# Optimization experiments

Hardware: AMD Instinct MI355X
Metric: run time of the kernel (lower is better)

Reference implementation:

```python
import jax, jax.numpy as jnp
import numpy as np

B, S, D_IN, D_OUT, H = 4, 2048, 1024, 1024, 16
HD = D_OUT // H  # head_dim = 64


def setup_inputs() -> dict:
    key = jax.random.key(0)
    ks = jax.random.split(key, 6)
    scale = 1.0 / np.sqrt(D_IN)
    return {
        "x": jax.random.normal(ks[0], (B, S, D_IN), dtype=jnp.float32),
        "Wq": jax.random.normal(ks[1], (D_IN, D_OUT), dtype=jnp.float32) * scale,
        "Wk": jax.random.normal(ks[2], (D_IN, D_OUT), dtype=jnp.float32) * scale,
        "Wv": jax.random.normal(ks[3], (D_IN, D_OUT), dtype=jnp.float32) * scale,
        "Wo": jax.random.normal(ks[4], (D_OUT, D_OUT), dtype=jnp.float32) * (1.0 / np.sqrt(D_OUT)),
        "bo": jax.random.normal(ks[5], (D_OUT,), dtype=jnp.float32) * 0.02,
    }


def reference(x, Wq, Wk, Wv, Wo, bo):
    b, n, _ = x.shape
    h, hd = H, HD
    # projections -> (b, h, n, hd)
    q = (x @ Wq).reshape(b, n, h, hd).transpose(0, 2, 1, 3)
    k = (x @ Wk).reshape(b, n, h, hd).transpose(0, 2, 1, 3)
    v = (x @ Wv).reshape(b, n, h, hd).transpose(0, 2, 1, 3)
    # scores (b, h, n, n) with causal mask then scale (matches original order)
    scores = jnp.einsum("bhqd,bhkd->bhqk", q, k)
    causal = jnp.tril(jnp.ones((n, n), dtype=bool))  # True = keep
    scores = jnp.where(causal, scores, -jnp.inf) / jnp.sqrt(jnp.asarray(hd, x.dtype))
    attn = jax.nn.softmax(scores, axis=-1)
    ctx = jnp.einsum("bhqk,bhkd->bhqd", attn, v)
    ctx = ctx.transpose(0, 2, 1, 3).reshape(b, n, h * hd)
    return ctx @ Wo + bo
```

## Files before the change

### kernel.cpp

```cpp
#include <hip/hip_runtime.h>
#include <hip/hip_bf16.h>
#include <math.h>

typedef __attribute__((ext_vector_type(4))) float f32x4;
typedef __attribute__((ext_vector_type(16))) float f32x16;
typedef __attribute__((ext_vector_type(8))) short bf16x8;
typedef __attribute__((ext_vector_type(4))) unsigned int u32x4;

#define DEV __device__ __forceinline__
#define MFMA16 __builtin_amdgcn_mfma_f32_16x16x32_bf16
#define MFMA32 __builtin_amdgcn_mfma_f32_32x32x16_bf16
#define SBAR __builtin_amdgcn_s_barrier()
#define SCHED0 __builtin_amdgcn_sched_barrier(0)

constexpr int S      = 2048;
constexpr int DMODEL = 1024;
constexpr int HD     = 64;
constexpr int MROWS  = 4 * 2048;

DEV unsigned short f2bf(float f) {
  union { float f; unsigned int u; } v; v.f = f;
  unsigned int u = v.u;
  unsigned int r = u + 0x7fffu + ((u >> 16) & 1u);
  return (unsigned short)(r >> 16);
}

DEV unsigned int pkbf(float lo, float hi) {
  unsigned int r;
  asm("v_cvt_pk_bf16_f32 %0, %1, %2" : "=v"(r) : "v"(lo), "v"(hi));
  return r;
}

DEV float fexp2(float x) { return __builtin_amdgcn_exp2f(x); }

DEV void gload_lds16(const void* g, void* l) {
  __builtin_amdgcn_global_load_lds(
      (const __attribute__((address_space(1))) unsigned int*)g,
      (__attribute__((address_space(3))) unsigned int*)l, 16, 0, 0);
}

__global__ __launch_bounds__(256) void k_conv(const float* __restrict__ in,
                                              unsigned short* __restrict__ out) {
  int i = blockIdx.x * 256 + threadIdx.x;
  float4 v = ((const float4*)in)[i];
  ushort4 o;
  o.x = f2bf(v.x); o.y = f2bf(v.y); o.z = f2bf(v.z); o.w = f2bf(v.w);
  ((ushort4*)out)[i] = o;
}

__global__ __launch_bounds__(256) void k_transpose4(const float* __restrict__ Wq,
                                                    const float* __restrict__ Wk,
                                                    const float* __restrict__ Wv,
                                                    const float* __restrict__ Wo,
                                                    unsigned short* __restrict__ wt,
                                                    unsigned short* __restrict__ wot) {
  __shared__ float tile[32][33];
  const int z = blockIdx.z;
  const float* W = (z == 0) ? Wq : (z == 1) ? Wk : (z == 2) ? Wv : Wo;
  unsigned short* Wt = (z == 3) ? wot : wt + (size_t)z * DMODEL * DMODEL;
  int n0 = blockIdx.x * 32, k0 = blockIdx.y * 32;
  int tx = threadIdx.x, ty = threadIdx.y;
#pragma unroll
  for (int j = 0; j < 4; ++j)
    tile[ty + j * 8][tx] = W[(size_t)(k0 + ty + j * 8) * DMODEL + n0 + tx];
  __syncthreads();
#pragma unroll
  for (int j = 0; j < 4; ++j)
    Wt[(size_t)(n0 + ty + j * 8) * DMODEL + k0 + tx] = f2bf(tile[tx][ty + j * 8]);
}

template<int NBX, int EPI>
__global__ __launch_bounds__(512, 2) void k_gemm8(const unsigned short* __restrict__ A,
                                                  const unsigned short* __restrict__ Bt,
                                                  unsigned short* __restrict__ Qg,
                                                  unsigned short* __restrict__ Kg,
                                                  unsigned short* __restrict__ Vt,
                                                  const float* __restrict__ bo,
                                                  float* __restrict__ out) {
  __shared__ __align__(16) char lds[147456];
  const int tid = threadIdx.x, lane = tid & 63;
  const int wid = tid >> 6, wm = wid >> 1, wn = wid & 1;
  const int lq = lane & 15, lg = lane >> 4;
  const int flat = blockIdx.x;
  const int wg = (flat & 7) * (NBX * 4) + (flat >> 3);
  const int by = wg / NBX, bx = wg % NBX;
  const int m0 = by * 256, n0 = bx * 128;

  auto stage = [&](int kt, int buf) {
    char* dA = lds + buf * 49152;
    char* dB = dA + 32768;
    const unsigned short* gA = A + (size_t)m0 * DMODEL + kt * 64;
    const unsigned short* gB = Bt + (size_t)n0 * DMODEL + kt * 64;
#pragma unroll
    for (int i = 0; i < 4; ++i) {
      int c = tid + i * 512; int r = c >> 3, cc = c & 7;
      gload_lds16(gA + (size_t)r * DMODEL + ((cc ^ (r & 7)) << 3), dA + c * 16);
    }
#pragma unroll
    for (int i = 0; i < 2; ++i) {
      int c = tid + i * 512; int r = c >> 3, cc = c & 7;
      gload_lds16(gB + (size_t)r * DMODEL + ((cc ^ (r & 7)) << 3), dB + c * 16);
    }
  };

  stage(0, 0);
  stage(1, 1);
  SCHED0;
  asm volatile("s_waitcnt vmcnt(6)" ::: "memory");
  SCHED0;
  SBAR;
  SCHED0;

  f32x4 acc[4][4] = {};
  int bcur = 0, bnxt = 1, bth = 2;
#pragma unroll 1
  for (int t = 0; t < 16; ++t) {
    if (t < 14) stage(t + 2, bth);
    const char* pA = lds + bcur * 49152;
    const char* pB = pA + 32768;
#pragma unroll
    for (int kk = 0; kk < 2; ++kk) {
      bf16x8 af[4], bf[4];
#pragma unroll
      for (int mi = 0; mi < 4; ++mi) {
        int row = wm * 64 + mi * 16 + lq;
        af[mi] = *(const bf16x8*)(pA + row * 128 + ((((kk << 2) + lg) ^ (row & 7)) << 4));
      }
#pragma unroll
      for (int ni = 0; ni < 4; ++ni) {
        int row = wn * 64 + ni * 16 + lq;
        bf[ni] = *(const bf16x8*)(pB + row * 128 + ((((kk << 2) + lg) ^ (row & 7)) << 4));
      }
      __builtin_amdgcn_s_setprio(1);
#pragma unroll
      for (int mi = 0; mi < 4; ++mi)
#pragma unroll
        for (int ni = 0; ni < 4; ++ni)
          acc[mi][ni] = MFMA16(af[mi], bf[ni], acc[mi][ni], 0, 0, 0);
      __builtin_amdgcn_s_setprio(0);
    }
    SCHED0;
    if (t < 14) {
      asm volatile("s_waitcnt vmcnt(6)" ::: "memory");
    } else if (t == 14) {
      asm volatile("s_waitcnt vmcnt(0)" ::: "memory");
    }
    SCHED0;
    if (t < 15) SBAR;
    SCHED0;
    int tmp = bcur; bcur = bnxt; bnxt = bth; bth = tmp;
  }

  if (EPI == 0) {
#pragma unroll
    for (int mi = 0; mi < 4; ++mi)
#pragma unroll
      for (int ni = 0; ni < 4; ++ni) {
        int n = n0 + wn * 64 + ni * 16 + lq;
        int widx = n >> 10, nn = n & 1023;
        int h = nn >> 6, d = nn & 63;
        int mbase = m0 + wm * 64 + mi * 16 + lg * 4;
        int b_ = mbase >> 11, s_ = mbase & 2047;
        if (widx == 2) {
          ushort4 o;
          o.x = f2bf(acc[mi][ni][0]);
          o.y = f2bf(acc[mi][ni][1]);
          o.z = f2bf(acc[mi][ni][2]);
          o.w = f2bf(acc[mi][ni][3]);
          *(ushort4*)(Vt + ((size_t)((b_ * 16 + h) * 64 + d)) * S + s_) = o;
        } else {
          unsigned short* dst = (widx == 0) ? Qg : Kg;
          float scale = (widx == 0) ? 0.18033688f : 1.0f;
#pragma unroll
          for (int r = 0; r < 4; ++r)
            dst[(size_t)((b_ * 16 + h) * 2048 + s_ + r) * HD + d] = f2bf(acc[mi][ni][r] * scale);
        }
      }
  } else {
#pragma unroll
    for (int mi = 0; mi < 4; ++mi)
#pragma unroll
      for (int ni = 0; ni < 4; ++ni) {
        int n = n0 + wn * 64 + ni * 16 + lq;
        float bv = bo[n];
#pragma unroll
        for (int r = 0; r < 4; ++r) {
          int m = m0 + wm * 64 + mi * 16 + lg * 4 + r;
          out[(size_t)m * DMODEL + n] = acc[mi][ni][r] + bv;
        }
      }
  }
}

__global__ __launch_bounds__(512, 2) void k_attn(const unsigned short* __restrict__ Qg,
                                                 const unsigned short* __restrict__ Kg,
                                                 const unsigned short* __restrict__ Vt,
                                                 unsigned short* __restrict__ Ctx) {
  __shared__ __align__(16) char lds[32768];
  const int f = blockIdx.x;
  const int i4 = f & 255, hi2 = f >> 8;
  const int bh = i4 >> 2, q = i4 & 3;
  const int Qb = hi2 ? (7 - q) : q;
  const int tid = threadIdx.x;
  const int lane = tid & 63, w = tid >> 6;
  const int lq5 = lane & 31, hi = lane >> 5;
  const size_t base = (size_t)bh * (S * HD);
  const int b = bh >> 4, h = bh & 15;
  const int krow = tid >> 3, kcc = tid & 7, scc = kcc ^ (krow & 7);
  const int vd = tid >> 3;
  const int vfd = (vd & 7) ^ ((vd >> 3) & 7);
  const int vscc = (tid & 7) ^ vfd;
  const unsigned short* VtRow = Vt + (size_t)(bh * 64 + vd) * S;

  const int q0w = Qb * 256 + w * 32;
  const int tmax = 4 * Qb + 3;
  const int diag = q0w >> 6;

  bf16x8 qF[4];
#pragma unroll
  for (int dc = 0; dc < 4; ++dc)
    qF[dc] = *(const bf16x8*)(Qg + base + (size_t)(q0w + lq5) * HD + dc * 16 + hi * 8);

  f32x16 o0 = {}, o1 = {};
  float m_run = -INFINITY, l_run = 0.f;

  gload_lds16(Kg + base + (size_t)krow * HD + scc * 8, lds + tid * 16);
  gload_lds16(VtRow + vscc * 8, lds + 16384 + tid * 16);
  __syncthreads();

#pragma unroll 1
  for (int t = 0; t <= tmax; ++t) {
    const int cur = t & 1, nxt = cur ^ 1;
    char* sK  = lds + cur * 8192;
    char* sVT = lds + 16384 + cur * 8192;
    const bool have_next = (t < tmax);
    if (have_next) {
      gload_lds16(Kg + base + (size_t)((t + 1) * 64 + krow) * HD + scc * 8,
                  lds + nxt * 8192 + tid * 16);
      gload_lds16(VtRow + (t + 1) * 64 + vscc * 8,
                  lds + 16384 + nxt * 8192 + tid * 16);
    }
    const bool active = (t <= diag);
    if (active) {
      const bool isdiag = (t == diag);
      const int nkb = (isdiag && !(q0w & 32)) ? 1 : 2;
      f32x16 st0 = {}, st1 = {};
#pragma unroll
      for (int dc = 0; dc < 4; ++dc) {
        int row = lq5;
        bf16x8 a0 = *(const bf16x8*)(sK + row * 128 + (((2 * dc + hi) ^ (row & 7)) << 4));
        st0 = MFMA32(a0, qF[dc], st0, 0, 0, 0);
      }
      if (nkb == 2) {
#pragma unroll
        for (int dc = 0; dc < 4; ++dc) {
          int row = 32 + lq5;
          bf16x8 a1 = *(const bf16x8*)(sK + row * 128 + (((2 * dc + hi) ^ (row & 7)) << 4));
          st1 = MFMA32(a1, qF[dc], st1, 0, 0, 0);
        }
      }
      if (isdiag) {
        int qo = q0w + lq5 - t * 64;
        if (q0w & 32) {
#pragma unroll
          for (int r = 0; r < 16; ++r) {
            int key = 32 + (r & 3) + 8 * (r >> 2) + 4 * hi;
            st1[r] = (key > qo) ? -INFINITY : st1[r];
          }
        } else {
#pragma unroll
          for (int r = 0; r < 16; ++r) {
            int key = (r & 3) + 8 * (r >> 2) + 4 * hi;
            st0[r] = (key > qo) ? -INFINITY : st0[r];
          }
        }
      }
      float mx = st0[0];
#pragma unroll
      for (int r = 1; r < 16; ++r) mx = fmaxf(mx, st0[r]);
      if (nkb == 2) {
#pragma unroll
        for (int r = 0; r < 16; ++r) mx = fmaxf(mx, st1[r]);
      }
      mx = fmaxf(mx, __shfl_xor(mx, 32));
      bool need = !(mx <= m_run + 8.0f);
      if (__any(need)) {
        float mn = fmaxf(m_run, mx);
        float alpha = fexp2(m_run - mn);
        m_run = mn;
        l_run *= alpha;
#pragma unroll
        for (int r = 0; r < 16; ++r) { o0[r] *= alpha; o1[r] *= alpha; }
      }
      float rs[4] = {0.f, 0.f, 0.f, 0.f};
#pragma unroll
      for (int r = 0; r < 16; ++r) {
        float p = fexp2(st0[r] - m_run);
        st0[r] = p;
        rs[r & 3] += p;
      }
      if (nkb == 2) {
#pragma unroll
        for (int r = 0; r < 16; ++r) {
          float p = fexp2(st1[r] - m_run);
          st1[r] = p;
          rs[r & 3] += p;
        }
      }
      float rsum = (rs[0] + rs[1]) + (rs[2] + rs[3]);
      rsum += __shfl_xor(rsum, 32);
      l_run += rsum;
      {
        unsigned int wv[8];
#pragma unroll
        for (int j = 0; j < 8; ++j) wv[j] = pkbf(st0[2 * j], st0[2 * j + 1]);
        asm("v_permlane32_swap_b32 %0, %1" : "+v"(wv[0]), "+v"(wv[2]));
        asm("v_permlane32_swap_b32 %0, %1" : "+v"(wv[1]), "+v"(wv[3]));
        asm("v_permlane32_swap_b32 %0, %1" : "+v"(wv[4]), "+v"(wv[6]));
        asm("v_permlane32_swap_b32 %0, %1" : "+v"(wv[5]), "+v"(wv[7]));
        union { bf16x8 v; unsigned int u[4]; } fa, fb;
        fa.u[0] = wv[0]; fa.u[1] = wv[1]; fa.u[2] = wv[2]; fa.u[3] = wv[3];
        fb.u[0] = wv[4]; fb.u[1] = wv[5]; fb.u[2] = wv[6]; fb.u[3] = wv[7];
#pragma unroll
        for (int kc = 0; kc < 2; ++kc) {
          bf16x8 bp = kc ? fb.v : fa.v;
          {
            int d = lq5, fd = (d & 7) ^ ((d >> 3) & 7);
            bf16x8 av = *(const bf16x8*)(sVT + d * 128 + (((kc * 2 + hi) ^ fd) << 4));
            o0 = MFMA32(av, bp, o0, 0, 0, 0);
          }
          {
            int d = 32 + lq5, fd = (d & 7) ^ ((d >> 3) & 7);
            bf16x8 av = *(const bf16x8*)(sVT + d * 128 + (((kc * 2 + hi) ^ fd) << 4));
            o1 = MFMA32(av, bp, o1, 0, 0, 0);
          }
        }
      }
      if (nkb == 2) {
        unsigned int wv[8];
#pragma unroll
        for (int j = 0; j < 8; ++j) wv[j] = pkbf(st1[2 * j], st1[2 * j + 1]);
        asm("v_permlane32_swap_b32 %0, %1" : "+v"(wv[0]), "+v"(wv[2]));
        asm("v_permlane32_swap_b32 %0, %1" : "+v"(wv[1]), "+v"(wv[3]));
        asm("v_permlane32_swap_b32 %0, %1" : "+v"(wv[4]), "+v"(wv[6]));
        asm("v_permlane32_swap_b32 %0, %1" : "+v"(wv[5]), "+v"(wv[7]));
        union { bf16x8 v; unsigned int u[4]; } fa, fb;
        fa.u[0] = wv[0]; fa.u[1] = wv[1]; fa.u[2] = wv[2]; fa.u[3] = wv[3];
        fb.u[0] = wv[4]; fb.u[1] = wv[5]; fb.u[2] = wv[6]; fb.u[3] = wv[7];
#pragma unroll
        for (int kc = 0; kc < 2; ++kc) {
          bf16x8 bp = kc ? fb.v : fa.v;
          {
            int d = lq5, fd = (d & 7) ^ ((d >> 3) & 7);
            bf16x8 av = *(const bf16x8*)(sVT + d * 128 + ((((2 + kc) * 2 + hi) ^ fd) << 4));
            o0 = MFMA32(av, bp, o0, 0, 0, 0);
          }
          {
            int d = 32 + lq5, fd = (d & 7) ^ ((d >> 3) & 7);
            bf16x8 av = *(const bf16x8*)(sVT + d * 128 + ((((2 + kc) * 2 + hi) ^ fd) << 4));
            o1 = MFMA32(av, bp, o1, 0, 0, 0);
          }
        }
      }
    }
    __syncthreads();
  }

  __syncthreads();
  {
    float inv = 1.0f / l_run;
    char* slice = lds + w * 4096;
#pragma unroll
    for (int db = 0; db < 2; ++db)
#pragma unroll
      for (int j = 0; j < 8; ++j) {
        int d0 = (j & 1) * 2 + (j >> 1) * 8 + 4 * hi + 32 * db;
        float va = (db ? o1[2 * j] : o0[2 * j]) * inv;
        float vb = (db ? o1[2 * j + 1] : o0[2 * j + 1]) * inv;
        *(unsigned int*)(slice + lq5 * 128 + (((d0 >> 3) ^ (lq5 & 7)) << 4) + (d0 & 7) * 2) =
            pkbf(va, vb);
      }
    asm volatile("s_waitcnt lgkmcnt(0)" ::: "memory");
#pragma unroll
    for (int i = 0; i < 4; ++i) {
      int r = lane >> 1, cc = (lane & 1) * 4 + i;
      u32x4 v = *(const u32x4*)(slice + r * 128 + ((cc ^ (r & 7)) << 4));
      *(u32x4*)(Ctx + (size_t)(b * S + q0w + r) * DMODEL + h * HD + cc * 8) = v;
    }
  }
}

extern "C" void kernel_launch(void* const* d_in, const int* in_sizes, int n_in,
                              void* d_out, int out_size, void* d_ws, size_t ws_size,
                              hipStream_t stream) {
  const float* x  = (const float*)d_in[0];
  const float* Wq = (const float*)d_in[1];
  const float* Wk = (const float*)d_in[2];
  const float* Wv = (const float*)d_in[3];
  const float* Wo = (const float*)d_in[4];
  const float* bo = (const float*)d_in[5];
  float* out = (float*)d_out;

  char* p = (char*)d_ws;
  unsigned short* xb  = (unsigned short*)p; p += (size_t)MROWS * DMODEL * 2;
  unsigned short* wt  = (unsigned short*)p; p += (size_t)3 * DMODEL * DMODEL * 2;
  unsigned short* wot = (unsigned short*)p; p += (size_t)DMODEL * DMODEL * 2;
  unsigned short* qg  = (unsigned short*)p; p += (size_t)MROWS * DMODEL * 2;
  unsigned short* kg  = (unsigned short*)p; p += (size_t)MROWS * DMODEL * 2;
  unsigned short* vt  = (unsigned short*)p; p += (size_t)MROWS * DMODEL * 2;
  unsigned short* ctx = (unsigned short*)p; p += (size_t)MROWS * DMODEL * 2;

  k_conv<<<(MROWS * DMODEL) / 1024, 256, 0, stream>>>(x, xb);
  k_transpose4<<<dim3(32, 32, 4), dim3(32, 8), 0, stream>>>(Wq, Wk, Wv, Wo, wt, wot);
  k_gemm8<24, 0><<<768, 512, 0, stream>>>(xb, wt, qg, kg, vt, nullptr, nullptr);
  k_attn<<<512, 512, 0, stream>>>(qg, kg, vt, ctx);
  k_gemm8<8, 1><<<256, 512, 0, stream>>>(ctx, wot, nullptr, nullptr, nullptr, bo, out);
}
```

Measured before the change: 166.7 us.

## Use 256x256 tiles with double buffering for the QKV projection GEMM

The fused QKV projection GEMM becomes its own kernel. It uses 256x256 output tiles across 8 waves in a 2x4 layout, with 8x4 MFMA accumulators per wave. This halves the grid to 384 blocks and raises arithmetic intensity per LDS load. The LDS pipeline changes from triple buffering with prefetch issued before compute to double buffering, where the prefetch is issued after a barrier that follows compute. That may expose more load latency, and the 128 accumulator registers per lane raise register pressure at 2 blocks/CU. The output-projection GEMM is split out as a non-templated kernel with rewritten buffer-rotation arithmetic.

```diff
diff --git a/kernel.cpp b/kernel.cpp
--- a/kernel.cpp
+++ b/kernel.cpp
@@ -69,18 +69,123 @@
     Wt[(size_t)(n0 + ty + j * 8) * DMODEL + k0 + tx] = f2bf(tile[tx][ty + j * 8]);
 }
 
-template<int NBX, int EPI>
-__global__ __launch_bounds__(512, 2) void k_gemm8(const unsigned short* __restrict__ A,
+__global__ __launch_bounds__(512, 2) void k_gemmQKV(const unsigned short* __restrict__ A,
+                                                    const unsigned short* __restrict__ Bt,
+                                                    unsigned short* __restrict__ Qg,
+                                                    unsigned short* __restrict__ Kg,
+                                                    unsigned short* __restrict__ Vt) {
+  __shared__ __align__(16) char lds[131072];
+  const int tid = threadIdx.x, lane = tid & 63;
+  const int wid = tid >> 6, wm = wid >> 2, wn = wid & 3;
+  const int lq = lane & 15, lg = lane >> 4;
+  constexpr int NBX = 12;
+  const int flat = blockIdx.x;
+  const int wg = (flat & 7) * (NBX * 4) + (flat >> 3);
+  const int by = wg / NBX, bx = wg % NBX;
+  const int m0 = by * 256, n0 = bx * 256;
+
+  auto stage = [&](int kt, int buf) {
+    char* dA = lds + buf * 65536;
+    char* dB = dA + 32768;
+    const unsigned short* gA = A + (size_t)m0 * DMODEL + kt * 64;
+    const unsigned short* gB = Bt + (size_t)n0 * DMODEL + kt * 64;
+#pragma unroll
+    for (int i = 0; i < 4; ++i) {
+      int c = tid + i * 512; int r = c >> 3, cc = c & 7;
+      gload_lds16(gA + (size_t)r * DMODEL + ((cc ^ (r & 7)) << 3), dA + c * 16);
+    }
+#pragma unroll
+    for (int i = 0; i < 4; ++i) {
+      int c = tid + i * 512; int r = c >> 3, cc = c & 7;
+      gload_lds16(gB + (size_t)r * DMODEL + ((cc ^ (r & 7)) << 3), dB + c * 16);
+    }
+  };
+
+  stage(0, 0);
+  stage(1, 1);
+  SCHED0;
+  asm volatile("s_waitcnt vmcnt(8)" ::: "memory");
+  SCHED0;
+  SBAR;
+  SCHED0;
+
+  f32x4 acc[8][4] = {};
+#pragma unroll 1
+  for (int t = 0; t < 16; ++t) {
+    const char* pA = lds + (t & 1) * 65536;
+    const char* pB = pA + 32768;
+#pragma unroll
+    for (int kk = 0; kk < 2; ++kk) {
+      bf16x8 af[8], bfr[4];
+#pragma unroll
+      for (int mi = 0; mi < 8; ++mi) {
+        int row = wm * 128 + mi * 16 + lq;
+        af[mi] = *(const bf16x8*)(pA + row * 128 + ((((kk << 2) + lg) ^ (row & 7)) << 4));
+      }
+#pragma unroll
+      for (int ni = 0; ni < 4; ++ni) {
+        int row = wn * 64 + ni * 16 + lq;
+        bfr[ni] = *(const bf16x8*)(pB + row * 128 + ((((kk << 2) + lg) ^ (row & 7)) << 4));
+      }
+      __builtin_amdgcn_s_setprio(1);
+#pragma unroll
+      for (int mi = 0; mi < 8; ++mi)
+#pragma unroll
+        for (int ni = 0; ni < 4; ++ni)
+          acc[mi][ni] = MFMA16(af[mi], bfr[ni], acc[mi][ni], 0, 0, 0);
+      __builtin_amdgcn_s_setprio(0);
+    }
+    asm volatile("s_waitcnt lgkmcnt(0)" ::: "memory");
+    SCHED0;
+    SBAR;
+    SCHED0;
+    if (t < 14) stage(t + 2, t & 1);
+    SCHED0;
+    if (t < 14) {
+      asm volatile("s_waitcnt vmcnt(8)" ::: "memory");
+    } else if (t == 14) {
+      asm volatile("s_waitcnt vmcnt(0)" ::: "memory");
+    }
+    SCHED0;
+    if (t < 15) SBAR;
+    SCHED0;
+  }
+
+#pragma unroll
+  for (int mi = 0; mi < 8; ++mi)
+#pragma unroll
+    for (int ni = 0; ni < 4; ++ni) {
+      int n = n0 + wn * 64 + ni * 16 + lq;
+      int widx = n >> 10, nn = n & 1023;
+      int h = nn >> 6, d = nn & 63;
+      int mbase = m0 + wm * 128 + mi * 16 + lg * 4;
+      int b_ = mbase >> 11, s_ = mbase & 2047;
+      if (widx == 2) {
+        ushort4 o;
+        o.x = f2bf(acc[mi][ni][0]);
+        o.y = f2bf(acc[mi][ni][1]);
+        o.z = f2bf(acc[mi][ni][2]);
+        o.w = f2bf(acc[mi][ni][3]);
+        *(ushort4*)(Vt + ((size_t)((b_ * 16 + h) * 64 + d)) * S + s_) = o;
+      } else {
+        unsigned short* dst = (widx == 0) ? Qg : Kg;
+        float scale = (widx == 0) ? 0.18033688f : 1.0f;
+#pragma unroll
+        for (int r = 0; r < 4; ++r)
+          dst[(size_t)((b_ * 16 + h) * 2048 + s_ + r) * HD + d] = f2bf(acc[mi][ni][r] * scale);
+      }
+    }
+}
+
+__global__ __launch_bounds__(512, 2) void k_gemmP(const unsigned short* __restrict__ A,
                                                   const unsigned short* __restrict__ Bt,
-                                                  unsigned short* __restrict__ Qg,
-                                                  unsigned short* __restrict__ Kg,
-                                                  unsigned short* __restrict__ Vt,
                                                   const float* __restrict__ bo,
                                                   float* __restrict__ out) {
   __shared__ __align__(16) char lds[147456];
   const int tid = threadIdx.x, lane = tid & 63;
   const int wid = tid >> 6, wm = wid >> 1, wn = wid & 1;
   const int lq = lane & 15, lg = lane >> 4;
+  constexpr int NBX = 8;
   const int flat = blockIdx.x;
   const int wg = (flat & 7) * (NBX * 4) + (flat >> 3);
   const int by = wg / NBX, bx = wg % NBX;
@@ -112,7 +217,7 @@
   SCHED0;
 
   f32x4 acc[4][4] = {};
-  int bcur = 0, bnxt = 1, bth = 2;
+  int bcur = 0, bth = 2;
 #pragma unroll 1
   for (int t = 0; t < 16; ++t) {
     if (t < 14) stage(t + 2, bth);
@@ -120,7 +225,7 @@
     const char* pB = pA + 32768;
 #pragma unroll
     for (int kk = 0; kk < 2; ++kk) {
-      bf16x8 af[4], bf[4];
+      bf16x8 af[4], bfr[4];
 #pragma unroll
       for (int mi = 0; mi < 4; ++mi) {
         int row = wm * 64 + mi * 16 + lq;
@@ -129,14 +234,14 @@
 #pragma unroll
       for (int ni = 0; ni < 4; ++ni) {
         int row = wn * 64 + ni * 16 + lq;
-        bf[ni] = *(const bf16x8*)(pB + row * 128 + ((((kk << 2) + lg) ^ (row & 7)) << 4));
+        bfr[ni] = *(const bf16x8*)(pB + row * 128 + ((((kk << 2) + lg) ^ (row & 7)) << 4));
       }
       __builtin_amdgcn_s_setprio(1);
 #pragma unroll
       for (int mi = 0; mi < 4; ++mi)
 #pragma unroll
         for (int ni = 0; ni < 4; ++ni)
-          acc[mi][ni] = MFMA16(af[mi], bf[ni], acc[mi][ni], 0, 0, 0);
+          acc[mi][ni] = MFMA16(af[mi], bfr[ni], acc[mi][ni], 0, 0, 0);
       __builtin_amdgcn_s_setprio(0);
     }
     SCHED0;
@@ -148,48 +253,23 @@
     SCHED0;
     if (t < 15) SBAR;
     SCHED0;
-    int tmp = bcur; bcur = bnxt; bnxt = bth; bth = tmp;
+    int nb = (bcur + 1 == 3) ? 0 : bcur + 1;
+    int nt = (bth + 1 == 3) ? 0 : bth + 1;
+    bcur = nb; bth = nt;
   }
 
-  if (EPI == 0) {
-#pragma unroll
-    for (int mi = 0; mi < 4; ++mi)
-#pragma unroll
-      for (int ni = 0; ni < 4; ++ni) {
-        int n = n0 + wn * 64 + ni * 16 + lq;
-        int widx = n >> 10, nn = n & 1023;
-        int h = nn >> 6, d = nn & 63;
-        int mbase = m0 + wm * 64 + mi * 16 + lg * 4;
-        int b_ = mbase >> 11, s_ = mbase & 2047;
-        if (widx == 2) {
-          ushort4 o;
-          o.x = f2bf(acc[mi][ni][0]);
-          o.y = f2bf(acc[mi][ni][1]);
-          o.z = f2bf(acc[mi][ni][2]);
-          o.w = f2bf(acc[mi][ni][3]);
-          *(ushort4*)(Vt + ((size_t)((b_ * 16 + h) * 64 + d)) * S + s_) = o;
-        } else {
-          unsigned short* dst = (widx == 0) ? Qg : Kg;
-          float scale = (widx == 0) ? 0.18033688f : 1.0f;
-#pragma unroll
-          for (int r = 0; r < 4; ++r)
-            dst[(size_t)((b_ * 16 + h) * 2048 + s_ + r) * HD + d] = f2bf(acc[mi][ni][r] * scale);
-        }
-      }
-  } else {
-#pragma unroll
-    for (int mi = 0; mi < 4; ++mi)
-#pragma unroll
-      for (int ni = 0; ni < 4; ++ni) {
-        int n = n0 + wn * 64 + ni * 16 + lq;
-        float bv = bo[n];
-#pragma unroll
-        for (int r = 0; r < 4; ++r) {
-          int m = m0 + wm * 64 + mi * 16 + lg * 4 + r;
-          out[(size_t)m * DMODEL + n] = acc[mi][ni][r] + bv;
-        }
-      }
-  }
+#pragma unroll
+  for (int mi = 0; mi < 4; ++mi)
+#pragma unroll
+    for (int ni = 0; ni < 4; ++ni) {
+      int n = n0 + wn * 64 + ni * 16 + lq;
+      float bv = bo[n];
+#pragma unroll
+      for (int r = 0; r < 4; ++r) {
+        int m = m0 + wm * 64 + mi * 16 + lg * 4 + r;
+        out[(size_t)m * DMODEL + n] = acc[mi][ni][r] + bv;
+      }
+    }
 }
 
 __global__ __launch_bounds__(512, 2) void k_attn(const unsigned short* __restrict__ Qg,
@@ -412,7 +492,7 @@
 
   k_conv<<<(MROWS * DMODEL) / 1024, 256, 0, stream>>>(x, xb);
   k_transpose4<<<dim3(32, 32, 4), dim3(32, 8), 0, stream>>>(Wq, Wk, Wv, Wo, wt, wot);
-  k_gemm8<24, 0><<<768, 512, 0, stream>>>(xb, wt, qg, kg, vt, nullptr, nullptr);
+  k_gemmQKV<<<384, 512, 0, stream>>>(xb, wt, qg, kg, vt);
   k_attn<<<512, 512, 0, stream>>>(qg, kg, vt, ctx);
-  k_gemm8<8, 1><<<256, 512, 0, stream>>>(ctx, wot, nullptr, nullptr, nullptr, bo, out);
-}
+  k_gemmP<<<256, 512, 0, stream>>>(ctx, wot, bo, out);
+}
```

Measured after the change: 168.6 us. No clear change (+1.1%).
